# Optimization experiments

Hardware: AMD Instinct MI355X
Metric: run time of the kernel (lower is better)

The kernel has to match this reference:

```python
import jax, jax.numpy as jnp
import numpy as np

KS, ST, SS, TOP_N, WIN = 32, 16, 64, 16, 512  # kernel_size, stride, select_size, top_n, window_size
NEG = -1e30


def setup_inputs() -> dict:
    key = jax.random.key(0)
    k0, k1, k2, k3 = jax.random.split(key, 4)
    B, S, H, Dqk, Dv = 1, 2048, 16, 128, 128
    q = jax.random.normal(k0, (B, S, H, Dqk), jnp.float32)
    k = jax.random.normal(k1, (B, S, H, Dqk), jnp.float32)
    v = jax.random.normal(k2, (B, S, H, Dv), jnp.float32)
    w_gate = jax.random.normal(k3, (Dqk, 3), jnp.float32) * (Dqk ** -0.5)
    b_gate = jnp.zeros((3,), jnp.float32)
    return {"q": q, "k": k, "v": v, "w_gate": w_gate, "b_gate": b_gate}


def _masked_probs(scores, mask):
    # numerically safe masked softmax; rows with no valid key yield all-zero probs
    s = jnp.where(mask, scores, NEG)
    lse = jax.nn.logsumexp(s, axis=-1, keepdims=True)
    return jnp.where(mask, jnp.exp(s - lse), 0.0)


def _nsa_forward(q, k, v, w_gate, b_gate):
    B, S, H, Dqk = q.shape
    scale = Dqk ** -0.5
    C = (S - KS) // ST + 1          # number of compressed blocks
    NSEL = S // SS                  # number of selection blocks
    tpos = jnp.arange(S)

    # ---- branch 1: compressed attention (mean-pooled K/V blocks) ----
    wpos = jnp.arange(C)[:, None] * ST + jnp.arange(KS)[None, :]   # [C,KS]
    cmp_k = k[:, wpos].mean(axis=2)                                # [B,C,H,Dqk]
    cmp_v = v[:, wpos].mean(axis=2)                                # [B,C,H,Dv]
    s_cmp = jnp.einsum('bqhd,bchd->bhqc', q, cmp_k) * scale
    cmp_end = jnp.arange(C) * ST + KS - 1
    cmask = cmp_end[None, :] <= tpos[:, None]                      # block fully in past
    p_cmp = _masked_probs(s_cmp, cmask)                            # [B,H,S,C]
    cmp_o = jnp.einsum('bhqc,bchd->bqhd', p_cmp, cmp_v)

    # ---- top-n block selection from compressed attention probs ----
    c_start = jnp.arange(C) * ST
    j_start = jnp.arange(NSEL) * SS
    overlap = ((c_start[:, None] < j_start[None, :] + SS) &
               (c_start[:, None] + KS > j_start[None, :])).astype(q.dtype)  # [C,NSEL]
    p_sel = jnp.einsum('bhqc,cj->bhqj', p_cmp, overlap)            # [B,H,S,NSEL]
    allowed = j_start[None, :] <= tpos[:, None]                    # block started
    cur_oh = jax.nn.one_hot(tpos // SS, NSEL, dtype=q.dtype)       # force current block
    sc = jnp.where(allowed, p_sel, -1.0) + 1e6 * cur_oh
    _, idx = jax.lax.top_k(sc, TOP_N)                              # [B,H,S,TOP_N]

    # ---- shared dense scores (reference only; real kernel is IO-aware) ----
    s_full = jnp.einsum('bqhd,bkhd->bhqk', q, k) * scale           # [B,H,S,S]
    causal = tpos[None, :] <= tpos[:, None]

    # ---- branch 2: selected-block attention ----
    blk_mask = (idx[..., None] == jnp.arange(NSEL)).any(axis=-2)   # [B,H,S,NSEL]
    key_blk = tpos // SS
    sel_mask = blk_mask[..., key_blk] & causal                     # [B,H,S,S]
    p_s = _masked_probs(s_full, sel_mask)
    select_o = jnp.einsum('bhqk,bkhd->bqhd', p_s, v)

    # ---- branch 3: sliding-window causal attention ----
    wmask = causal & ((tpos[:, None] - tpos[None, :]) <= WIN)
    p_w = _masked_probs(s_full, wmask)
    window_o = jnp.einsum('bhqk,bkhd->bqhd', p_w, v)

    # ---- learned per-query gates ----
    gate = jax.nn.sigmoid(jnp.einsum('bqhd,dg->bqhg', q, w_gate) + b_gate)
    return (cmp_o * gate[..., 0:1] + select_o * gate[..., 1:2]
            + window_o * gate[..., 2:3])


def reference(q, k, v, w_gate, b_gate):
    return _nsa_forward(q, k, v, w_gate, b_gate)
```

## Files before the change

### kernel.cpp

```cpp
#include <hip/hip_runtime.h>

#define S_LEN 2048
#define NH 16
#define DIM 128
#define KSZ 32
#define STRD 16
#define SSZ 64
#define NSELB 32
#define NCMP 127
#define TOPN 16
#define WINSZ 512
#define NEGF (-1e30f)
#define NEGTH (-1e29f)
#define SCALE 0.088388347648318447f

typedef __attribute__((ext_vector_type(8))) short bf16x8;
typedef __attribute__((ext_vector_type(4))) float f32x4;

__device__ __forceinline__ unsigned short f2bf(float f) {
  unsigned u = __builtin_bit_cast(unsigned, f);
  return (unsigned short)((u + 0x7FFFu + ((u >> 16) & 1u)) >> 16);
}
__device__ __forceinline__ float bf2f(unsigned short b) {
  return __builtin_bit_cast(float, (unsigned)b << 16);
}
__device__ __forceinline__ bf16x8 pack8(const float* f) {
  bf16x8 r;
#pragma unroll
  for (int i = 0; i < 8; ++i) r[i] = (short)f2bf(f[i]);
  return r;
}

#define SCIDX(r, c) ((r) * 132 + (((c) >> 5) * 33) + ((c) & 31))

__global__ __launch_bounds__(256) void nsa_build(
    const float* __restrict__ v, const float* __restrict__ k,
    unsigned short* __restrict__ vtg, unsigned short* __restrict__ kb) {
  const int c = blockIdx.x * 256 + threadIdx.x;
  {
    const int h = c >> 15, d = (c >> 8) & 127, tc = c & 255;
    float f[8];
#pragma unroll
    for (int i = 0; i < 8; ++i) f[i] = v[((tc * 8 + i) * NH + h) * DIM + d];
    *(bf16x8*)(vtg + ((h * DIM + d) * S_LEN + tc * 8)) = pack8(f);
  }
  {
    const int h = c >> 15, t = (c >> 4) & 2047, dc = c & 15;
    const float* src = k + ((t * NH + h) * DIM + dc * 8);
    float f[8];
#pragma unroll
    for (int i = 0; i < 8; ++i) f[i] = src[i];
    *(bf16x8*)(kb + ((h * S_LEN + t) * DIM + dc * 8)) = pack8(f);
  }
}

__global__ __launch_bounds__(128) void nsa_compress(
    const float* __restrict__ k, const float* __restrict__ v,
    unsigned short* __restrict__ cmpkh, unsigned short* __restrict__ cmpkl,
    unsigned short* __restrict__ cmpvt) {
  const int c = blockIdx.x & 127;
  const int h = blockIdx.x >> 7;
  const int d = threadIdx.x;
  float sk = 0.f, sv = 0.f;
  if (c < NCMP) {
    const int base = ((c * STRD) * NH + h) * DIM + d;
#pragma unroll
    for (int i = 0; i < KSZ; ++i) {
      sk += k[base + i * NH * DIM];
      sv += v[base + i * NH * DIM];
    }
    sk *= (1.0f / KSZ); sv *= (1.0f / KSZ);
  }
  const unsigned short hi = f2bf(sk);
  const unsigned short lo = f2bf(sk - bf2f(hi));
  cmpkh[(h * 128 + c) * 128 + d] = (c < NCMP) ? hi : 0;
  cmpkl[(h * 128 + c) * 128 + d] = (c < NCMP) ? lo : 0;
  cmpvt[(h * 128 + d) * 128 + c] = (c < NCMP) ? f2bf(sv) : 0;
}

__global__ __launch_bounds__(64, 2) void nsa_main(
    const float* __restrict__ q, const float* __restrict__ wg,
    const float* __restrict__ bg, const unsigned short* __restrict__ kb,
    const unsigned short* __restrict__ vtg,
    const unsigned short* __restrict__ cmpkh, const unsigned short* __restrict__ cmpkl,
    const unsigned short* __restrict__ cmpvt, float* __restrict__ out) {
  __shared__ float scw[16 * 132];
  __shared__ __align__(16) char pa[2112];
  __shared__ float gatesLds[48];
  __shared__ unsigned maskLds[16];

  const int b = blockIdx.x;
  const int h = ((b & 7) << 1) | ((b >> 3) & 1);
  const int tq0 = (127 - (b >> 4)) << 4;
  const int lane = threadIdx.x;
  const int l15 = lane & 15;
  const int l4 = lane >> 4;

  const int nvmax = tq0 >> 4;
  const int nct0 = (nvmax + 31) >> 5;
  const int nct = (nct0 < 4) ? nct0 : 4;

  if (lane < 16) maskLds[lane] = 0u;

  const unsigned short* kbh = kb + h * S_LEN * DIM;
  const unsigned short* vth = vtg + h * DIM * S_LEN;

  bf16x8 qfh[4];
  const float* qp = q + ((tq0 + l15) * NH + h) * DIM + l4 * 8;
#pragma unroll
  for (int ks = 0; ks < 4; ++ks) {
    float f[8];
#pragma unroll
    for (int i = 0; i < 8; ++i) f[i] = bf2f(f2bf(qp[ks * 32 + i]));
    qfh[ks] = pack8(f);
  }

  if (lane < 48) {
    const int qloc = lane / 3, gi = lane % 3;
    const float* qr_ = q + ((tq0 + qloc) * NH + h) * DIM;
    float acc = bg[gi];
#pragma unroll
    for (int d4 = 0; d4 < DIM; d4 += 4) {
      const float4 qv = *(const float4*)(qr_ + d4);
      acc += qv.x * wg[(d4 + 0) * 3 + gi] + qv.y * wg[(d4 + 1) * 3 + gi] +
             qv.z * wg[(d4 + 2) * 3 + gi] + qv.w * wg[(d4 + 3) * 3 + gi];
    }
    gatesLds[qloc * 3 + gi] = 1.0f / (1.0f + __expf(-acc));
  }

  {
    bf16x8 qfl[4];
#pragma unroll
    for (int ks = 0; ks < 4; ++ks) {
      float f[8];
#pragma unroll
      for (int i = 0; i < 8; ++i) {
        const float x = qp[ks * 32 + i];
        f[i] = x - bf2f(f2bf(x));
      }
      qfl[ks] = pack8(f);
    }
    for (int ct = 0; ct < nct; ++ct) {
      const unsigned short* bk = cmpkh + (h * 128 + ct * 32) * 128 + l4 * 8;
      const unsigned short* bkl = cmpkl + (h * 128 + ct * 32) * 128 + l4 * 8;
      f32x4 s0 = {0, 0, 0, 0}, s1 = {0, 0, 0, 0};
#pragma unroll
      for (int ks = 0; ks < 4; ++ks) {
        bf16x8 bh0 = *(const bf16x8*)(bk + l15 * 128 + ks * 32);
        bf16x8 bh1 = *(const bf16x8*)(bk + (16 + l15) * 128 + ks * 32);
        bf16x8 bl0 = *(const bf16x8*)(bkl + l15 * 128 + ks * 32);
        bf16x8 bl1 = *(const bf16x8*)(bkl + (16 + l15) * 128 + ks * 32);
        s0 = __builtin_amdgcn_mfma_f32_16x16x32_bf16(qfh[ks], bh0, s0, 0, 0, 0);
        s0 = __builtin_amdgcn_mfma_f32_16x16x32_bf16(qfl[ks], bh0, s0, 0, 0, 0);
        s0 = __builtin_amdgcn_mfma_f32_16x16x32_bf16(qfh[ks], bl0, s0, 0, 0, 0);
        s1 = __builtin_amdgcn_mfma_f32_16x16x32_bf16(qfh[ks], bh1, s1, 0, 0, 0);
        s1 = __builtin_amdgcn_mfma_f32_16x16x32_bf16(qfl[ks], bh1, s1, 0, 0, 0);
        s1 = __builtin_amdgcn_mfma_f32_16x16x32_bf16(qfh[ks], bl1, s1, 0, 0, 0);
      }
#pragma unroll
      for (int j = 0; j < 4; ++j) {
        const int qr = l4 * 4 + j;
        scw[SCIDX(qr, ct * 32 + l15)] = s0[j] * SCALE;
        scw[SCIDX(qr, ct * 32 + 16 + l15)] = s1[j] * SCALE;
      }
    }
  }

  {
    const int qq = lane >> 2, qg = lane & 3;
    const int tq = tq0 + qq;
    const int nv = (tq >= KSZ - 1) ? ((tq - (KSZ - 1)) / STRD + 1) : 0;
    float x[32];
#pragma unroll
    for (int i = 0; i < 32; ++i) x[i] = scw[SCIDX(qq, qg * 32 + i)];
    float m = NEGF;
#pragma unroll
    for (int i = 0; i < 32; ++i)
      if (qg * 32 + i < nv) m = fmaxf(m, x[i]);
    m = fmaxf(m, __shfl_xor(m, 1));
    m = fmaxf(m, __shfl_xor(m, 2));
    float s = 0.f;
#pragma unroll
    for (int i = 0; i < 32; ++i) {
      x[i] = (qg * 32 + i < nv) ? __expf(x[i] - m) : 0.f;
      s += x[i];
    }
    s += __shfl_xor(s, 1);
    s += __shfl_xor(s, 2);
    const float inv = (nv > 0) ? (1.0f / s) : 0.f;
#pragma unroll
    for (int i = 0; i < 32; ++i) scw[SCIDX(qq, qg * 32 + i)] = x[i] * inv;
  }

  {
    float* ssel = (float*)pa;
    const int qq = lane >> 2, jg = lane & 3;
    const int tq = tq0 + qq;
    float vj[8];
#pragma unroll
    for (int i = 0; i < 8; ++i) {
      const int j = jg * 8 + i;
      const int lo = (4 * j - 1 > 0) ? 4 * j - 1 : 0;
      const int hi = (4 * j + 3 < NCMP - 1) ? 4 * j + 3 : NCMP - 1;
      float ps = 0.f;
      for (int c = lo; c <= hi; ++c) ps += scw[SCIDX(qq, c)];
      float val = (j * SSZ <= tq) ? ps : -1.0f;
      if (j == (tq >> 6)) val += 1e6f;
      vj[i] = val;
      ssel[qq * 33 + j] = val;
    }
    float sv[32];
#pragma unroll
    for (int jp = 0; jp < 32; ++jp) sv[jp] = ssel[qq * 33 + jp];
#pragma unroll
    for (int i = 0; i < 8; ++i) {
      const int j = jg * 8 + i;
      const float my = vj[i];
      int rank = 0;
#pragma unroll
      for (int jp = 0; jp < 32; ++jp)
        rank += (sv[jp] > my) || (sv[jp] == my && jp < j);
      if (rank < TOPN && (j * SSZ <= tq)) atomicOr(&maskLds[qq], 1u << j);
    }
  }

  unsigned maskq[4];
#pragma unroll
  for (int j = 0; j < 4; ++j) maskq[j] = maskLds[l4 * 4 + j];
  unsigned sel16 = maskq[0] | maskq[1] | maskq[2] | maskq[3];
  sel16 |= __shfl_xor(sel16, 16);
  sel16 |= __shfl_xor(sel16, 32);

  {
    f32x4 accC[8];
#pragma unroll
    for (int n = 0; n < 8; ++n) accC[n] = (f32x4){0, 0, 0, 0};
    for (int ct = 0; ct < nct; ++ct) {
      float f[8];
#pragma unroll
      for (int i = 0; i < 8; ++i) f[i] = scw[SCIDX(l15, ct * 32 + l4 * 8 + i)];
      bf16x8 ap = pack8(f);
      const unsigned short* cvb = cmpvt + (h * 128) * 128 + ct * 32 + l4 * 8;
#pragma unroll
      for (int n = 0; n < 8; ++n) {
        bf16x8 bvv = *(const bf16x8*)(cvb + (n * 16 + l15) * 128);
        accC[n] = __builtin_amdgcn_mfma_f32_16x16x32_bf16(ap, bvv, accC[n], 0, 0, 0);
      }
    }
#pragma unroll
    for (int j = 0; j < 4; ++j) {
      const int qr = l4 * 4 + j;
      const float g0 = gatesLds[qr * 3 + 0];
#pragma unroll
      for (int n = 0; n < 8; ++n) scw[SCIDX(qr, n * 16 + l15)] = g0 * accC[n][j];
    }
  }

  f32x4 accS[8], accW[8];
#pragma unroll
  for (int n = 0; n < 8; ++n) { accS[n] = (f32x4){0, 0, 0, 0}; accW[n] = (f32x4){0, 0, 0, 0}; }
  float mS[4], lS[4], mW[4], lW[4];
#pragma unroll
  for (int j = 0; j < 4; ++j) { mS[j] = NEGF; lS[j] = 0.f; mW[j] = NEGF; lW[j] = 0.f; }

  char* paS = pa;
  char* paW = pa + 1024;
  const int ktmax = (tq0 + 15) >> 5;
  const int winlo = tq0 - WINSZ;

  for (int kt = 0; kt <= ktmax; ++kt) {
    const int kt0 = kt << 5;
    const int jb = kt >> 1;
    const bool selAct = (sel16 >> jb) & 1u;
    const bool winAct = (kt0 + 31) >= winlo;
    if (!selAct && !winAct) continue;

    const unsigned short* kbase = kbh + kt0 * DIM + l4 * 8;
    f32x4 s0 = {0, 0, 0, 0}, s1 = {0, 0, 0, 0};
#pragma unroll
    for (int ks = 0; ks < 4; ++ks) {
      bf16x8 b0 = *(const bf16x8*)(kbase + l15 * DIM + ks * 32);
      bf16x8 b1 = *(const bf16x8*)(kbase + (16 + l15) * DIM + ks * 32);
      s0 = __builtin_amdgcn_mfma_f32_16x16x32_bf16(qfh[ks], b0, s0, 0, 0, 0);
      s1 = __builtin_amdgcn_mfma_f32_16x16x32_bf16(qfh[ks], b1, s1, 0, 0, 0);
    }
    bf16x8 bv[8];
    const unsigned short* vbase = vth + kt0 + l4 * 8;
#pragma unroll
    for (int n = 0; n < 8; ++n)
      bv[n] = *(const bf16x8*)(vbase + (n * 16 + l15) * S_LEN);

    const int c0 = kt0 + l15, c1 = kt0 + 16 + l15;
#pragma unroll
    for (int j = 0; j < 4; ++j) {
      const int qr = l4 * 4 + j;
      const int tq = tq0 + qr;
      const float sv0 = s0[j] * SCALE, sv1 = s1[j] * SCALE;
      if (selAct) {
        const bool mb = (maskq[j] >> jb) & 1u;
        const float v0 = (mb && c0 <= tq) ? sv0 : NEGF;
        const float v1 = (mb && c1 <= tq) ? sv1 : NEGF;
        const float rml = fmaxf(v0, v1);
        if (__any(rml > mS[j] + 8.0f)) {
          float rm = rml;
          rm = fmaxf(rm, __shfl_xor(rm, 1));
          rm = fmaxf(rm, __shfl_xor(rm, 2));
          rm = fmaxf(rm, __shfl_xor(rm, 4));
          rm = fmaxf(rm, __shfl_xor(rm, 8));
          if (rm > mS[j]) {
            const float sf = __expf(mS[j] - rm);
            lS[j] *= sf;
#pragma unroll
            for (int n = 0; n < 8; ++n) accS[n][j] *= sf;
            mS[j] = rm;
          }
        }
        const float p0 = (v0 > NEGTH) ? __expf(v0 - mS[j]) : 0.f;
        const float p1 = (v1 > NEGTH) ? __expf(v1 - mS[j]) : 0.f;
        lS[j] += p0 + p1;
        *(unsigned short*)(paS + qr * 64 + ((l15 * 2) ^ (j << 4))) = f2bf(p0);
        *(unsigned short*)(paS + qr * 64 + (((16 + l15) * 2) ^ (j << 4))) = f2bf(p1);
      }
      if (winAct) {
        const float v0 = (c0 <= tq && c0 >= tq - WINSZ) ? sv0 : NEGF;
        const float v1 = (c1 <= tq && c1 >= tq - WINSZ) ? sv1 : NEGF;
        const float rml = fmaxf(v0, v1);
        if (__any(rml > mW[j] + 8.0f)) {
          float rm = rml;
          rm = fmaxf(rm, __shfl_xor(rm, 1));
          rm = fmaxf(rm, __shfl_xor(rm, 2));
          rm = fmaxf(rm, __shfl_xor(rm, 4));
          rm = fmaxf(rm, __shfl_xor(rm, 8));
          if (rm > mW[j]) {
            const float sf = __expf(mW[j] - rm);
            lW[j] *= sf;
#pragma unroll
            for (int n = 0; n < 8; ++n) accW[n][j] *= sf;
            mW[j] = rm;
          }
        }
        const float p0 = (v0 > NEGTH) ? __expf(v0 - mW[j]) : 0.f;
        const float p1 = (v1 > NEGTH) ? __expf(v1 - mW[j]) : 0.f;
        lW[j] += p0 + p1;
        *(unsigned short*)(paW + qr * 64 + ((l15 * 2) ^ (j << 4))) = f2bf(p0);
        *(unsigned short*)(paW + qr * 64 + (((16 + l15) * 2) ^ (j << 4))) = f2bf(p1);
      }
    }
    if (selAct) {
      bf16x8 ap = *(const bf16x8*)(paS + l15 * 64 + ((l4 * 16) ^ ((l15 & 3) << 4)));
#pragma unroll
      for (int n = 0; n < 8; ++n)
        accS[n] = __builtin_amdgcn_mfma_f32_16x16x32_bf16(ap, bv[n], accS[n], 0, 0, 0);
    }
    if (winAct) {
      bf16x8 ap = *(const bf16x8*)(paW + l15 * 64 + ((l4 * 16) ^ ((l15 & 3) << 4)));
#pragma unroll
      for (int n = 0; n < 8; ++n)
        accW[n] = __builtin_amdgcn_mfma_f32_16x16x32_bf16(ap, bv[n], accW[n], 0, 0, 0);
    }
  }

#pragma unroll
  for (int j = 0; j < 4; ++j) {
    float ls = lS[j], lw = lW[j];
    ls += __shfl_xor(ls, 1); lw += __shfl_xor(lw, 1);
    ls += __shfl_xor(ls, 2); lw += __shfl_xor(lw, 2);
    ls += __shfl_xor(ls, 4); lw += __shfl_xor(lw, 4);
    ls += __shfl_xor(ls, 8); lw += __shfl_xor(lw, 8);
    const int qr = l4 * 4 + j;
    const int tq = tq0 + qr;
    const float rlS = gatesLds[qr * 3 + 1] / ls;
    const float rlW = gatesLds[qr * 3 + 2] / lw;
#pragma unroll
    for (int n = 0; n < 8; ++n)
      out[(tq * NH + h) * DIM + n * 16 + l15] =
          scw[SCIDX(qr, n * 16 + l15)] + accS[n][j] * rlS + accW[n][j] * rlW;
  }
}

extern "C" void kernel_launch(void* const* d_in, const int* in_sizes, int n_in,
                              void* d_out, int out_size, void* d_ws, size_t ws_size,
                              hipStream_t stream) {
  const float* q  = (const float*)d_in[0];
  const float* k  = (const float*)d_in[1];
  const float* v  = (const float*)d_in[2];
  const float* wg = (const float*)d_in[3];
  const float* bg = (const float*)d_in[4];
  float* out = (float*)d_out;

  unsigned short* vtg   = (unsigned short*)d_ws;
  unsigned short* kb    = vtg + NH * DIM * S_LEN;
  unsigned short* cmpkh = kb + NH * S_LEN * DIM;
  unsigned short* cmpkl = cmpkh + NH * 128 * 128;
  unsigned short* cmpvt = cmpkl + NH * 128 * 128;

  nsa_build<<<2048, 256, 0, stream>>>(v, k, vtg, kb);
  nsa_compress<<<NH * 128, 128, 0, stream>>>(k, v, cmpkh, cmpkl, cmpvt);
  nsa_main<<<2048, 64, 0, stream>>>(q, wg, bg, kb, vtg, cmpkh, cmpkl, cmpvt, out);
}
```

Measured before the change: 231.3 us.

## Iterate active key tiles via bitmask, prefetch next K tile, use exp2 softmax

After: 229.3 us. Within noise of the previous version (-0.9%).

```diff
diff --git a/kernel.cpp b/kernel.cpp
--- a/kernel.cpp
+++ b/kernel.cpp
@@ -13,6 +13,7 @@
 #define NEGF (-1e30f)
 #define NEGTH (-1e29f)
 #define SCALE 0.088388347648318447f
+#define SCALE2 (0.088388347648318447f * 1.4426950408889634f)
 
 typedef __attribute__((ext_vector_type(8))) short bf16x8;
 typedef __attribute__((ext_vector_type(4))) float f32x4;
@@ -256,6 +257,23 @@
     }
   }
 
+  const int ktmax = (tq0 + 15) >> 5;
+  const int ktw = (tq0 > WINSZ) ? ((tq0 - WINSZ) >> 5) : 0;
+  unsigned long long actmask;
+  {
+    unsigned long long m = (unsigned long long)sel16;
+    m = (m | (m << 16)) & 0x0000FFFF0000FFFFull;
+    m = (m | (m << 8))  & 0x00FF00FF00FF00FFull;
+    m = (m | (m << 4))  & 0x0F0F0F0F0F0F0F0Full;
+    m = (m | (m << 2))  & 0x3333333333333333ull;
+    m = (m | (m << 1))  & 0x5555555555555555ull;
+    const unsigned long long em = m * 3ull;
+    const unsigned long long winm = ~0ull << ktw;
+    const unsigned long long rng =
+        (ktmax >= 63) ? ~0ull : ((1ull << (ktmax + 1)) - 1ull);
+    actmask = (em | winm) & rng;
+  }
+
   f32x4 accS[8], accW[8];
 #pragma unroll
   for (int n = 0; n < 8; ++n) { accS[n] = (f32x4){0, 0, 0, 0}; accW[n] = (f32x4){0, 0, 0, 0}; }
@@ -265,58 +283,78 @@
 
   char* paS = pa;
   char* paW = pa + 1024;
-  const int ktmax = (tq0 + 15) >> 5;
-  const int winlo = tq0 - WINSZ;
-
-  for (int kt = 0; kt <= ktmax; ++kt) {
+
+  unsigned long long rem = actmask;
+  int kt = rem ? __builtin_ctzll(rem) : 0;
+  bf16x8 kf[8];
+  if (rem) {
+    const unsigned short* kbase = kbh + (kt << 5) * DIM + l4 * 8;
+#pragma unroll
+    for (int ks = 0; ks < 4; ++ks) {
+      kf[ks] = *(const bf16x8*)(kbase + l15 * DIM + ks * 32);
+      kf[4 + ks] = *(const bf16x8*)(kbase + (16 + l15) * DIM + ks * 32);
+    }
+  }
+
+  while (rem) {
+    rem &= rem - 1ull;
     const int kt0 = kt << 5;
     const int jb = kt >> 1;
     const bool selAct = (sel16 >> jb) & 1u;
-    const bool winAct = (kt0 + 31) >= winlo;
-    if (!selAct && !winAct) continue;
-
-    const unsigned short* kbase = kbh + kt0 * DIM + l4 * 8;
+    const bool winAct = kt >= ktw;
+    const int ktn = rem ? __builtin_ctzll(rem) : -1;
+
+    __builtin_amdgcn_s_setprio(1);
     f32x4 s0 = {0, 0, 0, 0}, s1 = {0, 0, 0, 0};
 #pragma unroll
     for (int ks = 0; ks < 4; ++ks) {
-      bf16x8 b0 = *(const bf16x8*)(kbase + l15 * DIM + ks * 32);
-      bf16x8 b1 = *(const bf16x8*)(kbase + (16 + l15) * DIM + ks * 32);
-      s0 = __builtin_amdgcn_mfma_f32_16x16x32_bf16(qfh[ks], b0, s0, 0, 0, 0);
-      s1 = __builtin_amdgcn_mfma_f32_16x16x32_bf16(qfh[ks], b1, s1, 0, 0, 0);
-    }
+      s0 = __builtin_amdgcn_mfma_f32_16x16x32_bf16(qfh[ks], kf[ks], s0, 0, 0, 0);
+      s1 = __builtin_amdgcn_mfma_f32_16x16x32_bf16(qfh[ks], kf[4 + ks], s1, 0, 0, 0);
+    }
+    __builtin_amdgcn_s_setprio(0);
+
     bf16x8 bv[8];
     const unsigned short* vbase = vth + kt0 + l4 * 8;
 #pragma unroll
     for (int n = 0; n < 8; ++n)
       bv[n] = *(const bf16x8*)(vbase + (n * 16 + l15) * S_LEN);
+
+    if (ktn >= 0) {
+      const unsigned short* kbase = kbh + (ktn << 5) * DIM + l4 * 8;
+#pragma unroll
+      for (int ks = 0; ks < 4; ++ks) {
+        kf[ks] = *(const bf16x8*)(kbase + l15 * DIM + ks * 32);
+        kf[4 + ks] = *(const bf16x8*)(kbase + (16 + l15) * DIM + ks * 32);
+      }
+    }
 
     const int c0 = kt0 + l15, c1 = kt0 + 16 + l15;
 #pragma unroll
     for (int j = 0; j < 4; ++j) {
       const int qr = l4 * 4 + j;
       const int tq = tq0 + qr;
-      const float sv0 = s0[j] * SCALE, sv1 = s1[j] * SCALE;
+      const float sv0 = s0[j] * SCALE2, sv1 = s1[j] * SCALE2;
       if (selAct) {
         const bool mb = (maskq[j] >> jb) & 1u;
         const float v0 = (mb && c0 <= tq) ? sv0 : NEGF;
         const float v1 = (mb && c1 <= tq) ? sv1 : NEGF;
         const float rml = fmaxf(v0, v1);
-        if (__any(rml > mS[j] + 8.0f)) {
+        if (__any(rml > mS[j] + 11.5416541f)) {
           float rm = rml;
           rm = fmaxf(rm, __shfl_xor(rm, 1));
           rm = fmaxf(rm, __shfl_xor(rm, 2));
           rm = fmaxf(rm, __shfl_xor(rm, 4));
           rm = fmaxf(rm, __shfl_xor(rm, 8));
           if (rm > mS[j]) {
-            const float sf = __expf(mS[j] - rm);
+            const float sf = exp2f(mS[j] - rm);
             lS[j] *= sf;
 #pragma unroll
             for (int n = 0; n < 8; ++n) accS[n][j] *= sf;
             mS[j] = rm;
           }
         }
-        const float p0 = (v0 > NEGTH) ? __expf(v0 - mS[j]) : 0.f;
-        const float p1 = (v1 > NEGTH) ? __expf(v1 - mS[j]) : 0.f;
+        const float p0 = (v0 > NEGTH) ? exp2f(v0 - mS[j]) : 0.f;
+        const float p1 = (v1 > NEGTH) ? exp2f(v1 - mS[j]) : 0.f;
         lS[j] += p0 + p1;
         *(unsigned short*)(paS + qr * 64 + ((l15 * 2) ^ (j << 4))) = f2bf(p0);
         *(unsigned short*)(paS + qr * 64 + (((16 + l15) * 2) ^ (j << 4))) = f2bf(p1);
@@ -325,27 +363,28 @@
         const float v0 = (c0 <= tq && c0 >= tq - WINSZ) ? sv0 : NEGF;
         const float v1 = (c1 <= tq && c1 >= tq - WINSZ) ? sv1 : NEGF;
         const float rml = fmaxf(v0, v1);
-        if (__any(rml > mW[j] + 8.0f)) {
+        if (__any(rml > mW[j] + 11.5416541f)) {
           float rm = rml;
           rm = fmaxf(rm, __shfl_xor(rm, 1));
           rm = fmaxf(rm, __shfl_xor(rm, 2));
           rm = fmaxf(rm, __shfl_xor(rm, 4));
           rm = fmaxf(rm, __shfl_xor(rm, 8));
           if (rm > mW[j]) {
-            const float sf = __expf(mW[j] - rm);
+            const float sf = exp2f(mW[j] - rm);
             lW[j] *= sf;
 #pragma unroll
             for (int n = 0; n < 8; ++n) accW[n][j] *= sf;
             mW[j] = rm;
           }
         }
-        const float p0 = (v0 > NEGTH) ? __expf(v0 - mW[j]) : 0.f;
-        const float p1 = (v1 > NEGTH) ? __expf(v1 - mW[j]) : 0.f;
+        const float p0 = (v0 > NEGTH) ? exp2f(v0 - mW[j]) : 0.f;
+        const float p1 = (v1 > NEGTH) ? exp2f(v1 - mW[j]) : 0.f;
         lW[j] += p0 + p1;
         *(unsigned short*)(paW + qr * 64 + ((l15 * 2) ^ (j << 4))) = f2bf(p0);
         *(unsigned short*)(paW + qr * 64 + (((16 + l15) * 2) ^ (j << 4))) = f2bf(p1);
       }
     }
+    __builtin_amdgcn_s_setprio(1);
     if (selAct) {
       bf16x8 ap = *(const bf16x8*)(paS + l15 * 64 + ((l4 * 16) ^ ((l15 & 3) << 4)));
 #pragma unroll
@@ -358,6 +397,8 @@
       for (int n = 0; n < 8; ++n)
         accW[n] = __builtin_amdgcn_mfma_f32_16x16x32_bf16(ap, bv[n], accW[n], 0, 0, 0);
     }
+    __builtin_amdgcn_s_setprio(0);
+    kt = ktn;
   }
 
 #pragma unroll
```
